# Kernel tuning notes

Hardware: AMD Instinct MI355X
Metric: run time of the kernel (lower is better)

Reference implementation:

```python
import jax, jax.numpy as jnp
import numpy as np

ALPHA = 0.9
EPS = 1e-12
INIT_VALS = (0.001, 0.0001)


def setup_inputs() -> dict:
    key = jax.random.key(0)
    x = jax.random.normal(key, (16, 2000, 481, 2), dtype=jnp.float32)
    return {"x": x}


def reference(x):
    # x: [B, T, F, 2] (real/imag)
    B, T, F, _ = x.shape
    step = (INIT_VALS[1] - INIT_VALS[0]) / (F - 1)
    s0 = INIT_VALS[0] + jnp.arange(F, dtype=x.dtype) * step  # [F]
    s0 = jnp.broadcast_to(s0[None, :], (B, F))               # [B, F]

    x_abs = jnp.sqrt(x[..., 0] ** 2 + x[..., 1] ** 2)        # [B, T, F]

    def ema_step(s, xa_t):
        # s, xa_t: [B, F]
        s = ALPHA * s + (1.0 - ALPHA) * xa_t
        inv = 1.0 / jnp.sqrt(s + EPS)
        return s, inv

    # scan over time axis: move T to front
    _, inv = jax.lax.scan(ema_step, s0, jnp.moveaxis(x_abs, 1, 0))  # inv: [T, B, F]
    inv = jnp.moveaxis(inv, 0, 1)                                   # [B, T, F]

    # normalize both real and imag parts by the same rsqrt(s + eps)
    return x * inv[..., None]  # [B, T, F, 2]
```

## Files before the change

kernel.cpp:

```cpp
#include <hip/hip_runtime.h>
#include <math.h>


#define ALPHA 0.9f
#define ONE_MINUS_ALPHA 0.1f
#define EPS_ 1e-12f

typedef float vf2 __attribute__((ext_vector_type(2)));

constexpr int B = 16;
constexpr int T = 2000;
constexpr int F = 481;
constexpr int NCH = 16;
constexpr int CHUNK = T / NCH;
constexpr int LOOKBACK = 128;

__global__ __launch_bounds__(64)
void specnorm_kernel(const float* __restrict__ x, float* __restrict__ out) {
    const int f = blockIdx.x * 64 + threadIdx.x;
    if (f >= F) return;
    const int chunk = blockIdx.y;
    const int b = blockIdx.z;

    const float step = (float)((0.0001 - 0.001) / (double)(F - 1));
    float s = 0.001f + (float)f * step;

    const int t0 = chunk * CHUNK;
    int tstart = t0 - LOOKBACK;
    if (tstart < 0) tstart = 0;

    const vf2* __restrict__ xp = (const vf2*)x;
    vf2* __restrict__ op = (vf2*)out;

    size_t idx = ((size_t)b * T + (size_t)tstart) * F + f;

    #pragma unroll 8
    for (int t = tstart; t < t0; ++t) {
        vf2 v = xp[idx];
        float xa = sqrtf(v.x * v.x + v.y * v.y);
        s = ALPHA * s + ONE_MINUS_ALPHA * xa;
        idx += F;
    }

    #pragma unroll 8
    for (int t = 0; t < CHUNK; ++t) {
        vf2 v = xp[idx];
        float xa = sqrtf(v.x * v.x + v.y * v.y);
        s = ALPHA * s + ONE_MINUS_ALPHA * xa;
        float inv = rsqrtf(s + EPS_);
        vf2 o;
        o.x = v.x * inv;
        o.y = v.y * inv;
        __builtin_nontemporal_store(o, &op[idx]);
        idx += F;
    }
}

extern "C" void kernel_launch(void* const* d_in, const int* in_sizes, int n_in,
                              void* d_out, int out_size, void* d_ws, size_t ws_size,
                              hipStream_t stream) {
    const float* x = (const float*)d_in[0];
    float* out = (float*)d_out;

    dim3 grid((F + 63) / 64, NCH, B);
    dim3 block(64);
    specnorm_kernel<<<grid, block, 0, stream>>>(x, out);
}
```

Before: 253.2 us.

## Process two frequency bins per thread with 16-byte loads and balanced chunks

Remaps work so that each block covers a whole frequency row for one batch. Each thread handles two adjacent frequency bins with a single 16-byte load, and the final odd bin's second lane writes into workspace as a dummy target. Time chunks are now uneven: the first chunk needs no warmup and does more output steps, which balances serial work across chunks. Hardware sqrt and rsq intrinsics replace the library calls. The grid shrinks to 256 blocks of 256 threads, which cuts total threads and may lower latency hiding. The last thread's vector load also reads a little past its row.

New measurement: 246.6 us. -2.6%, faster.

```diff
diff --git a/kernel.cpp b/kernel.cpp
--- a/kernel.cpp
+++ b/kernel.cpp
@@ -3,56 +3,66 @@
 
 
 #define ALPHA 0.9f
-#define ONE_MINUS_ALPHA 0.1f
-#define EPS_ 1e-12f
+#define OMA   0.1f
+#define EPS_  1e-12f
 
-typedef float vf2 __attribute__((ext_vector_type(2)));
+typedef float vf4 __attribute__((ext_vector_type(4), aligned(8)));
+typedef float vf2 __attribute__((ext_vector_type(2), aligned(8)));
 
-constexpr int B = 16;
-constexpr int T = 2000;
-constexpr int F = 481;
-constexpr int NCH = 16;
-constexpr int CHUNK = T / NCH;
-constexpr int LOOKBACK = 128;
+constexpr int B_ = 16, T_ = 2000, F_ = 481;
+constexpr int NCH = 16, LOOKBACK = 128;
+constexpr int OUT0 = 245, OUTN = 117;
+constexpr int ROWF = 2 * F_;
 
-__global__ __launch_bounds__(64)
-void specnorm_kernel(const float* __restrict__ x, float* __restrict__ out) {
-    const int f = blockIdx.x * 64 + threadIdx.x;
-    if (f >= F) return;
-    const int chunk = blockIdx.y;
-    const int b = blockIdx.z;
+__global__ __launch_bounds__(256)
+void specnorm_kernel(const float* __restrict__ x, float* __restrict__ out,
+                     float* __restrict__ ws) {
+    const int tid = threadIdx.x;
+    if (tid > 240) return;
+    const int chunk = blockIdx.x;
+    const int b = blockIdx.y;
+    const bool hasB = (tid < 240);
 
-    const float step = (float)((0.0001 - 0.001) / (double)(F - 1));
-    float s = 0.001f + (float)f * step;
+    const float step = (float)((0.0001 - 0.001) / (double)(F_ - 1));
+    float sA = 0.001f + (float)(2 * tid) * step;
+    float sB = 0.001f + (float)(2 * tid + 1) * step;
 
-    const int t0 = chunk * CHUNK;
-    int tstart = t0 - LOOKBACK;
-    if (tstart < 0) tstart = 0;
+    const int tout0 = (chunk == 0) ? 0 : OUT0 + (chunk - 1) * OUTN;
+    const int nout  = (chunk == 0) ? OUT0 : OUTN;
+    const int nwarm = (chunk == 0) ? 0 : LOOKBACK;
+    const int tstart = tout0 - nwarm;
 
-    const vf2* __restrict__ xp = (const vf2*)x;
-    vf2* __restrict__ op = (vf2*)out;
-
-    size_t idx = ((size_t)b * T + (size_t)tstart) * F + f;
+    const float* xp = x + (size_t)(b * T_ + tstart) * ROWF + 4 * tid;
+    float* opA = out + (size_t)(b * T_ + tout0) * ROWF + 4 * tid;
+    float* opB = hasB ? (opA + 2) : (ws + 2 * (size_t)tid);
+    const ptrdiff_t strideB = hasB ? ROWF : 0;
 
     #pragma unroll 8
-    for (int t = tstart; t < t0; ++t) {
-        vf2 v = xp[idx];
-        float xa = sqrtf(v.x * v.x + v.y * v.y);
-        s = ALPHA * s + ONE_MINUS_ALPHA * xa;
-        idx += F;
+    for (int t = 0; t < nwarm; ++t) {
+        vf4 v = *(const vf4*)xp;
+        float aA = __builtin_amdgcn_sqrtf(v.x * v.x + v.y * v.y);
+        float aB = __builtin_amdgcn_sqrtf(v.z * v.z + v.w * v.w);
+        sA = ALPHA * sA + OMA * aA;
+        sB = ALPHA * sB + OMA * aB;
+        xp += ROWF;
     }
 
     #pragma unroll 8
-    for (int t = 0; t < CHUNK; ++t) {
-        vf2 v = xp[idx];
-        float xa = sqrtf(v.x * v.x + v.y * v.y);
-        s = ALPHA * s + ONE_MINUS_ALPHA * xa;
-        float inv = rsqrtf(s + EPS_);
-        vf2 o;
-        o.x = v.x * inv;
-        o.y = v.y * inv;
-        __builtin_nontemporal_store(o, &op[idx]);
-        idx += F;
+    for (int t = 0; t < nout; ++t) {
+        vf4 v = *(const vf4*)xp;
+        float aA = __builtin_amdgcn_sqrtf(v.x * v.x + v.y * v.y);
+        float aB = __builtin_amdgcn_sqrtf(v.z * v.z + v.w * v.w);
+        sA = ALPHA * sA + OMA * aA;
+        sB = ALPHA * sB + OMA * aB;
+        float iA = __builtin_amdgcn_rsqf(sA + EPS_);
+        float iB = __builtin_amdgcn_rsqf(sB + EPS_);
+        vf2 oA = { v.x * iA, v.y * iA };
+        vf2 oB = { v.z * iB, v.w * iB };
+        __builtin_nontemporal_store(oA, (vf2*)opA);
+        __builtin_nontemporal_store(oB, (vf2*)opB);
+        xp += ROWF;
+        opA += ROWF;
+        opB += strideB;
     }
 }
 
@@ -61,8 +71,9 @@
                               hipStream_t stream) {
     const float* x = (const float*)d_in[0];
     float* out = (float*)d_out;
+    float* ws = (float*)d_ws;
 
-    dim3 grid((F + 63) / 64, NCH, B);
-    dim3 block(64);
-    specnorm_kernel<<<grid, block, 0, stream>>>(x, out);
+    dim3 grid(NCH, B_);
+    dim3 block(256);
+    specnorm_kernel<<<grid, block, 0, stream>>>(x, out, ws);
 }
```
